# Performance work log

Hardware: AMD Instinct MI355X
Metric: run time of the kernel (lower is better)

## Reference

```python
import jax, jax.numpy as jnp
import numpy as np

DIM = 2048
N_HEADS = 16
HEAD_DIM = DIM // N_HEADS
HIDDEN = 8192
BATCH = 2
SEQ = 2048
EPS = 1e-6


def setup_inputs() -> dict:
    key = jax.random.key(0)
    ks = jax.random.split(key, 10)
    x = jax.random.normal(ks[0], (BATCH, SEQ, DIM), dtype=jnp.float32)
    # standard RoPE angles: theta_j = 10000^{-2j/head_dim}, angle = pos * theta_j
    inv_freq = 1.0 / (10000.0 ** (np.arange(0, HEAD_DIM, 2, dtype=np.float32) / HEAD_DIM))
    angles = np.arange(SEQ, dtype=np.float32)[:, None] * inv_freq[None, :]  # [S, HD/2]
    freqs_cos = jnp.asarray(np.cos(angles))
    freqs_sin = jnp.asarray(np.sin(angles))
    # causal mask added to scores
    mask = jnp.where(jnp.tril(jnp.ones((SEQ, SEQ), dtype=bool)), 0.0, -jnp.inf)[None, None].astype(jnp.float32)
    s = 0.02
    wq = jax.random.normal(ks[1], (DIM, DIM), jnp.float32) * s
    wk = jax.random.normal(ks[2], (DIM, DIM), jnp.float32) * s
    wv = jax.random.normal(ks[3], (DIM, DIM), jnp.float32) * s
    wo = jax.random.normal(ks[4], (DIM, DIM), jnp.float32) * s
    w1 = jax.random.normal(ks[5], (DIM, HIDDEN), jnp.float32) * s
    w2 = jax.random.normal(ks[6], (HIDDEN, DIM), jnp.float32) * s
    w3 = jax.random.normal(ks[7], (DIM, HIDDEN), jnp.float32) * s
    attn_norm_w = jnp.ones((DIM,), jnp.float32)
    ffn_norm_w = jnp.ones((DIM,), jnp.float32)
    return {"x": x, "freqs_cos": freqs_cos, "freqs_sin": freqs_sin, "mask": mask,
            "wq": wq, "wk": wk, "wv": wv, "wo": wo, "w1": w1, "w2": w2, "w3": w3,
            "attn_norm_w": attn_norm_w, "ffn_norm_w": ffn_norm_w}


def _rmsnorm(x, w):
    xf = x.astype(jnp.float32)
    y = xf * jax.lax.rsqrt(jnp.mean(xf * xf, axis=-1, keepdims=True) + EPS)
    return y.astype(x.dtype) * w


def _rope(t, cos, sin):
    # t: [B,S,H,HD]; complex mult on adjacent pairs
    tr = t.astype(jnp.float32).reshape(*t.shape[:-1], HEAD_DIM // 2, 2)
    a, b = tr[..., 0], tr[..., 1]
    c = cos[None, :, None, :]  # [1,S,1,HD/2]
    s = sin[None, :, None, :]
    out = jnp.stack([a * c - b * s, a * s + b * c], axis=-1)
    return out.reshape(t.shape).astype(t.dtype)


def reference(x, freqs_cos, freqs_sin, mask, wq, wk, wv, wo, w1, w2, w3, attn_norm_w, ffn_norm_w):
    B, S, D = x.shape
    xn = _rmsnorm(x, attn_norm_w)
    q = (xn @ wq).reshape(B, S, N_HEADS, HEAD_DIM)
    k = (xn @ wk).reshape(B, S, N_HEADS, HEAD_DIM)
    v = (xn @ wv).reshape(B, S, N_HEADS, HEAD_DIM)
    q = _rope(q, freqs_cos, freqs_sin)
    k = _rope(k, freqs_cos, freqs_sin)
    scale = 1.0 / jnp.sqrt(jnp.float32(HEAD_DIM))
    scores = jnp.einsum('bqhd,bkhd->bhqk', q, k) * scale + mask
    probs = jax.nn.softmax(scores.astype(jnp.float32), axis=-1).astype(q.dtype)
    attn = jnp.einsum('bhqk,bkhd->bqhd', probs, v).reshape(B, S, D)
    h = x + attn @ wo
    hn = _rmsnorm(h, ffn_norm_w)
    ff = (jax.nn.silu(hn @ w1) * (hn @ w3)) @ w2
    return h + ff
```

## Files before the change

### kernel.cpp

```cpp
#include <hip/hip_runtime.h>
#include <cmath>

#define DIM    2048
#define NHEADS 16
#define HD     128
#define HIDDEN 8192
#define SEQ    2048
#define MTOK   4096
#define EPS    1e-6f

typedef __bf16 bf16;
typedef __bf16 bf16x8 __attribute__((ext_vector_type(8)));
typedef __bf16 bf16x4 __attribute__((ext_vector_type(4)));
typedef float  f32x4  __attribute__((ext_vector_type(4)));

__global__ void k_transpose_bf16(const float* __restrict__ in, bf16* __restrict__ out,
                                 int R, int C) {
    __shared__ float tile[32][33];
    int r0 = blockIdx.y * 32, c0 = blockIdx.x * 32;
    int tx = threadIdx.x, ty = threadIdx.y;
#pragma unroll
    for (int i = ty; i < 32; i += 8)
        tile[i][tx] = in[(size_t)(r0 + i) * C + (c0 + tx)];
    __syncthreads();
#pragma unroll
    for (int i = ty; i < 32; i += 8)
        out[(size_t)(c0 + i) * R + (r0 + tx)] = (bf16)tile[tx][i];
}

__global__ void k_rmsnorm(const float* __restrict__ x, const float* __restrict__ w,
                          bf16* __restrict__ out) {
    int row = blockIdx.x;
    int tid = threadIdx.x;
    const float4* xr = (const float4*)(x + (size_t)row * DIM);
    float4 a = xr[tid];
    float4 b = xr[tid + 256];
    float ss = a.x*a.x + a.y*a.y + a.z*a.z + a.w*a.w
             + b.x*b.x + b.y*b.y + b.z*b.z + b.w*b.w;
#pragma unroll
    for (int off = 32; off > 0; off >>= 1) ss += __shfl_down(ss, off, 64);
    __shared__ float red[4];
    if ((tid & 63) == 0) red[tid >> 6] = ss;
    __syncthreads();
    float tot = red[0] + red[1] + red[2] + red[3];
    float inv = rsqrtf(tot * (1.0f / DIM) + EPS);
    const float4* wr = (const float4*)w;
    float4 w0 = wr[tid], w1 = wr[tid + 256];
    bf16x4* o = (bf16x4*)(out + (size_t)row * DIM);
    bf16x4 v0, v1;
    v0[0] = (bf16)(a.x * inv * w0.x); v0[1] = (bf16)(a.y * inv * w0.y);
    v0[2] = (bf16)(a.z * inv * w0.z); v0[3] = (bf16)(a.w * inv * w0.w);
    v1[0] = (bf16)(b.x * inv * w1.x); v1[1] = (bf16)(b.y * inv * w1.y);
    v1[2] = (bf16)(b.z * inv * w1.z); v1[3] = (bf16)(b.w * inv * w1.w);
    o[tid] = v0;
    o[tid + 256] = v1;
}

__global__ void k_rope(bf16* __restrict__ qb, bf16* __restrict__ kb,
                       const float* __restrict__ fcos, const float* __restrict__ fsin) {
    bf16* t = blockIdx.y ? kb : qb;
    int idx = blockIdx.x * 256 + threadIdx.x;
    int m = idx >> 10;
    int p = idx & 1023;
    int i = p & 63;
    int col = (p >> 6) * HD + 2 * i;
    int pos = m & (SEQ - 1);
    float c = fcos[pos * 64 + i], s = fsin[pos * 64 + i];
    size_t off = (size_t)m * DIM + col;
    float a = (float)t[off], b = (float)t[off + 1];
    t[off]     = (bf16)(a * c - b * s);
    t[off + 1] = (bf16)(a * s + b * c);
}

template<int DUAL, int RESID, int OUT_F32>
__global__ __launch_bounds__(256, 2) void k_gemm(
    const bf16* __restrict__ A, const bf16* __restrict__ B1,
    const bf16* __restrict__ B2, const float* __restrict__ resid,
    void* __restrict__ outp, int M, int N, int K)
{
    __shared__ bf16 As [128][72];
    __shared__ bf16 Bs1[128][72];
    __shared__ bf16 Bs2[DUAL ? 128 : 1][72];

    const int tid  = threadIdx.x;
    const int wid  = tid >> 6;
    const int lane = tid & 63;
    const int quad = lane >> 4;
    const int l16  = lane & 15;
    const int wm   = wid >> 1;
    const int wn   = wid & 1;
    const int m0   = blockIdx.y * 128;
    const int n0   = blockIdx.x * 128;
    const int tr   = tid >> 3;
    const int tc   = (tid & 7) * 8;

    f32x4 acc1[4][4] = {};
    f32x4 acc2[4][4] = {};

    const int nk = K >> 6;
    for (int kt = 0; kt < nk; ++kt) {
        const int k0 = kt << 6;
        __syncthreads();
#pragma unroll
        for (int p = 0; p < 4; ++p) {
            int row = p * 32 + tr;
            *(uint4*)&As [row][tc] = *(const uint4*)&A [(size_t)(m0 + row) * K + k0 + tc];
            *(uint4*)&Bs1[row][tc] = *(const uint4*)&B1[(size_t)(n0 + row) * K + k0 + tc];
            if (DUAL)
                *(uint4*)&Bs2[row][tc] = *(const uint4*)&B2[(size_t)(n0 + row) * K + k0 + tc];
        }
        __syncthreads();
#pragma unroll
        for (int kk = 0; kk < 64; kk += 32) {
            bf16x8 af[4], bf1[4], bf2[4];
#pragma unroll
            for (int i = 0; i < 4; ++i) {
                af[i]  = *(const bf16x8*)&As [wm * 64 + i * 16 + l16][kk + quad * 8];
                bf1[i] = *(const bf16x8*)&Bs1[wn * 64 + i * 16 + l16][kk + quad * 8];
                if (DUAL)
                    bf2[i] = *(const bf16x8*)&Bs2[wn * 64 + i * 16 + l16][kk + quad * 8];
            }
#pragma unroll
            for (int mi = 0; mi < 4; ++mi)
#pragma unroll
                for (int ni = 0; ni < 4; ++ni) {
                    acc1[mi][ni] = __builtin_amdgcn_mfma_f32_16x16x32_bf16(
                        af[mi], bf1[ni], acc1[mi][ni], 0, 0, 0);
                    if (DUAL)
                        acc2[mi][ni] = __builtin_amdgcn_mfma_f32_16x16x32_bf16(
                            af[mi], bf2[ni], acc2[mi][ni], 0, 0, 0);
                }
        }
    }

#pragma unroll
    for (int mi = 0; mi < 4; ++mi)
#pragma unroll
        for (int i = 0; i < 4; ++i) {
            int row = m0 + wm * 64 + mi * 16 + quad * 4 + i;
#pragma unroll
            for (int ni = 0; ni < 4; ++ni) {
                int col = n0 + wn * 64 + ni * 16 + l16;
                float v1 = acc1[mi][ni][i];
                if (DUAL) {
                    float v2 = acc2[mi][ni][i];
                    float g = v1 / (1.0f + __expf(-v1));
                    ((bf16*)outp)[(size_t)row * N + col] = (bf16)(g * v2);
                } else if (OUT_F32) {
                    float r = RESID ? resid[(size_t)row * N + col] : 0.0f;
                    ((float*)outp)[(size_t)row * N + col] = r + v1;
                } else {
                    ((bf16*)outp)[(size_t)row * N + col] = (bf16)v1;
                }
            }
        }
}

__global__ __launch_bounds__(256, 2) void k_flash(
    const bf16* __restrict__ q, const bf16* __restrict__ k,
    const bf16* __restrict__ v, bf16* __restrict__ o)
{
    const int qt = 15 - blockIdx.x;
    const int bh = blockIdx.y;
    const int b  = bh >> 4, h = bh & 15;
    const int tid  = threadIdx.x;
    const int wid  = tid >> 6, lane = tid & 63;
    const int quad = lane >> 4, l16 = lane & 15;

    __shared__ bf16 Ks [128][136];
    __shared__ bf16 Vts[128][136];

    const int q0 = qt * 128;
    const size_t baseQ  = ((size_t)b * SEQ + q0) * DIM + (size_t)h * HD;
    const size_t baseKV = ((size_t)b * SEQ) * DIM + (size_t)h * HD;

    bf16x8 qf[2][4];
#pragma unroll
    for (int mi = 0; mi < 2; ++mi)
#pragma unroll
        for (int ks = 0; ks < 4; ++ks)
            qf[mi][ks] = *(const bf16x8*)&q[baseQ +
                (size_t)(wid * 32 + mi * 16 + l16) * DIM + ks * 32 + quad * 8];

    f32x4 acc_o[2][8] = {};
    float m_run[2][4], l_run[2][4];
#pragma unroll
    for (int mi = 0; mi < 2; ++mi)
#pragma unroll
        for (int i = 0; i < 4; ++i) { m_run[mi][i] = -INFINITY; l_run[mi][i] = 0.f; }

    const float scale = 0.08838834764831845f;
    const int krow = tid >> 1, kcol = (tid & 1) * 64;

    for (int kt = 0; kt <= qt; ++kt) {
        const int kbase = kt * 128;
        __syncthreads();
#pragma unroll
        for (int j = 0; j < 8; ++j)
            *(uint4*)&Ks[krow][kcol + j * 8] =
                *(const uint4*)&k[baseKV + (size_t)(kbase + krow) * DIM + kcol + j * 8];
#pragma unroll
        for (int j = 0; j < 8; ++j) {
            bf16x8 vv = *(const bf16x8*)&v[baseKV + (size_t)(kbase + krow) * DIM + kcol + j * 8];
#pragma unroll
            for (int e = 0; e < 8; ++e)
                Vts[kcol + j * 8 + e][krow] = vv[e];
        }
        __syncthreads();

        f32x4 accs[2][8] = {};
#pragma unroll
        for (int ks = 0; ks < 4; ++ks)
#pragma unroll
            for (int ni = 0; ni < 8; ++ni) {
                bf16x8 kf = *(const bf16x8*)&Ks[ni * 16 + l16][ks * 32 + quad * 8];
#pragma unroll
                for (int mi = 0; mi < 2; ++mi)
                    accs[mi][ni] = __builtin_amdgcn_mfma_f32_16x16x32_bf16(
                        qf[mi][ks], kf, accs[mi][ni], 0, 0, 0);
            }

#pragma unroll
        for (int mi = 0; mi < 2; ++mi)
#pragma unroll
            for (int i = 0; i < 4; ++i) {
                int grow = q0 + wid * 32 + mi * 16 + quad * 4 + i;
                float mx = -INFINITY;
#pragma unroll
                for (int ni = 0; ni < 8; ++ni) {
                    float sv = accs[mi][ni][i] * scale;
                    int col = kbase + ni * 16 + l16;
                    if (col > grow) sv = -INFINITY;
                    accs[mi][ni][i] = sv;
                    mx = fmaxf(mx, sv);
                }
                mx = fmaxf(mx, __shfl_xor(mx, 1, 64));
                mx = fmaxf(mx, __shfl_xor(mx, 2, 64));
                mx = fmaxf(mx, __shfl_xor(mx, 4, 64));
                mx = fmaxf(mx, __shfl_xor(mx, 8, 64));
                float mnew  = fmaxf(m_run[mi][i], mx);
                float alpha = __expf(m_run[mi][i] - mnew);
                m_run[mi][i] = mnew;
                float rsum = 0.f;
#pragma unroll
                for (int ni = 0; ni < 8; ++ni) {
                    float p = __expf(accs[mi][ni][i] - mnew);
                    accs[mi][ni][i] = p;
                    rsum += p;
                }
                rsum += __shfl_xor(rsum, 1, 64);
                rsum += __shfl_xor(rsum, 2, 64);
                rsum += __shfl_xor(rsum, 4, 64);
                rsum += __shfl_xor(rsum, 8, 64);
                l_run[mi][i] = l_run[mi][i] * alpha + rsum;
#pragma unroll
                for (int ni = 0; ni < 8; ++ni) acc_o[mi][ni][i] *= alpha;
            }

        __syncthreads();
#pragma unroll
        for (int mi = 0; mi < 2; ++mi)
#pragma unroll
            for (int ni = 0; ni < 8; ++ni)
#pragma unroll
                for (int i = 0; i < 4; ++i)
                    Ks[wid * 32 + mi * 16 + quad * 4 + i][ni * 16 + l16] =
                        (bf16)accs[mi][ni][i];
        __syncthreads();

#pragma unroll
        for (int ks2 = 0; ks2 < 4; ++ks2) {
            bf16x8 pf[2];
#pragma unroll
            for (int mi = 0; mi < 2; ++mi)
                pf[mi] = *(const bf16x8*)&Ks[wid * 32 + mi * 16 + l16][ks2 * 32 + quad * 8];
#pragma unroll
            for (int ni = 0; ni < 8; ++ni) {
                bf16x8 vf = *(const bf16x8*)&Vts[ni * 16 + l16][ks2 * 32 + quad * 8];
#pragma unroll
                for (int mi = 0; mi < 2; ++mi)
                    acc_o[mi][ni] = __builtin_amdgcn_mfma_f32_16x16x32_bf16(
                        pf[mi], vf, acc_o[mi][ni], 0, 0, 0);
            }
        }
    }

#pragma unroll
    for (int mi = 0; mi < 2; ++mi)
#pragma unroll
        for (int i = 0; i < 4; ++i) {
            float invl = 1.0f / l_run[mi][i];
            int row = q0 + wid * 32 + mi * 16 + quad * 4 + i;
            size_t rb = ((size_t)b * SEQ + row) * DIM + (size_t)h * HD;
#pragma unroll
            for (int ni = 0; ni < 8; ++ni)
                o[rb + ni * 16 + l16] = (bf16)(acc_o[mi][ni][i] * invl);
        }
}

extern "C" void kernel_launch(void* const* d_in, const int* in_sizes, int n_in,
                              void* d_out, int out_size, void* d_ws, size_t ws_size,
                              hipStream_t stream)
{
    (void)in_sizes; (void)n_in; (void)out_size; (void)ws_size;
    const float* x    = (const float*)d_in[0];
    const float* fcos = (const float*)d_in[1];
    const float* fsin = (const float*)d_in[2];
    const float* wq   = (const float*)d_in[4];
    const float* wk   = (const float*)d_in[5];
    const float* wv   = (const float*)d_in[6];
    const float* wo   = (const float*)d_in[7];
    const float* w1   = (const float*)d_in[8];
    const float* w2   = (const float*)d_in[9];
    const float* w3   = (const float*)d_in[10];
    const float* anw  = (const float*)d_in[11];
    const float* fnw  = (const float*)d_in[12];
    float* out = (float*)d_out;

    char* ws = (char*)d_ws;
    size_t off = 0;
    auto alloc = [&](size_t bytes) { void* p = ws + off; off += (bytes + 255) & ~255ull; return p; };
    bf16* wqT = (bf16*)alloc((size_t)DIM * DIM * 2);
    bf16* wkT = (bf16*)alloc((size_t)DIM * DIM * 2);
    bf16* wvT = (bf16*)alloc((size_t)DIM * DIM * 2);
    bf16* woT = (bf16*)alloc((size_t)DIM * DIM * 2);
    bf16* w1T = (bf16*)alloc((size_t)HIDDEN * DIM * 2);
    bf16* w3T = (bf16*)alloc((size_t)HIDDEN * DIM * 2);
    bf16* xn  = (bf16*)alloc((size_t)MTOK * DIM * 2);
    bf16* qb  = (bf16*)alloc((size_t)MTOK * DIM * 2);
    bf16* kb  = (bf16*)alloc((size_t)MTOK * DIM * 2);
    bf16* vb  = (bf16*)alloc((size_t)MTOK * DIM * 2);
    bf16* ffb = (bf16*)alloc((size_t)MTOK * HIDDEN * 2);
    bf16* w2T = kb;

    dim3 tb(32, 8);
    k_transpose_bf16<<<dim3(DIM / 32, DIM / 32), tb, 0, stream>>>(wq, wqT, DIM, DIM);
    k_transpose_bf16<<<dim3(DIM / 32, DIM / 32), tb, 0, stream>>>(wk, wkT, DIM, DIM);
    k_transpose_bf16<<<dim3(DIM / 32, DIM / 32), tb, 0, stream>>>(wv, wvT, DIM, DIM);
    k_transpose_bf16<<<dim3(DIM / 32, DIM / 32), tb, 0, stream>>>(wo, woT, DIM, DIM);
    k_transpose_bf16<<<dim3(HIDDEN / 32, DIM / 32), tb, 0, stream>>>(w1, w1T, DIM, HIDDEN);
    k_transpose_bf16<<<dim3(HIDDEN / 32, DIM / 32), tb, 0, stream>>>(w3, w3T, DIM, HIDDEN);

    k_rmsnorm<<<MTOK, 256, 0, stream>>>(x, anw, xn);

    dim3 g2k(DIM / 128, MTOK / 128);
    k_gemm<0, 0, 0><<<g2k, 256, 0, stream>>>(xn, wqT, nullptr, nullptr, qb, MTOK, DIM, DIM);
    k_gemm<0, 0, 0><<<g2k, 256, 0, stream>>>(xn, wkT, nullptr, nullptr, kb, MTOK, DIM, DIM);
    k_gemm<0, 0, 0><<<g2k, 256, 0, stream>>>(xn, wvT, nullptr, nullptr, vb, MTOK, DIM, DIM);

    k_rope<<<dim3((MTOK * 1024) / 256, 2), 256, 0, stream>>>(qb, kb, fcos, fsin);

    k_flash<<<dim3(SEQ / 128, 2 * NHEADS), 256, 0, stream>>>(qb, kb, vb, qb);

    k_transpose_bf16<<<dim3(DIM / 32, HIDDEN / 32), tb, 0, stream>>>(w2, w2T, HIDDEN, DIM);

    k_gemm<0, 1, 1><<<g2k, 256, 0, stream>>>(qb, woT, nullptr, x, out, MTOK, DIM, DIM);

    k_rmsnorm<<<MTOK, 256, 0, stream>>>(out, fnw, xn);

    k_gemm<1, 0, 0><<<dim3(HIDDEN / 128, MTOK / 128), 256, 0, stream>>>(
        xn, w1T, w3T, nullptr, ffb, MTOK, HIDDEN, DIM);

    k_gemm<0, 1, 1><<<g2k, 256, 0, stream>>>(ffb, w2T, nullptr, out, out, MTOK, DIM, HIDDEN);
}
```

Baseline: 1.241 ms.

## Fuse QKV GEMMs with RoPE epilogue, use direct global-to-LDS loads in GEMM

Replaces the three separate Q/K/V GEMMs and the standalone RoPE kernel with one GEMM over the concatenated transposed weights. RoPE is applied in the epilogue, using a lane shuffle to pair adjacent columns. The GEMM tile loads now use global_load_lds to write straight into unpadded LDS, and launch bounds are raised to allow more resident blocks. The weight transpose moves to 64x64 tiles. This cuts launches, the extra read-modify-write pass over Q/K, and register staging, at the risk of LDS bank conflicts from the unpadded rows. It also relies on the Q/K/V weight buffers being contiguous in the workspace.

```diff
diff --git a/kernel.cpp b/kernel.cpp
--- a/kernel.cpp
+++ b/kernel.cpp
@@ -14,17 +14,22 @@
 typedef __bf16 bf16x4 __attribute__((ext_vector_type(4)));
 typedef float  f32x4  __attribute__((ext_vector_type(4)));
 
+__device__ __forceinline__ void gl_lds16(const void* g, void* l) {
+    __builtin_amdgcn_global_load_lds((const __attribute__((address_space(1))) void*)g,
+                                     (__attribute__((address_space(3))) void*)l, 16, 0, 0);
+}
+
 __global__ void k_transpose_bf16(const float* __restrict__ in, bf16* __restrict__ out,
                                  int R, int C) {
-    __shared__ float tile[32][33];
-    int r0 = blockIdx.y * 32, c0 = blockIdx.x * 32;
+    __shared__ float tile[64][65];
+    int r0 = blockIdx.y * 64, c0 = blockIdx.x * 64;
     int tx = threadIdx.x, ty = threadIdx.y;
 #pragma unroll
-    for (int i = ty; i < 32; i += 8)
+    for (int i = ty; i < 64; i += 4)
         tile[i][tx] = in[(size_t)(r0 + i) * C + (c0 + tx)];
     __syncthreads();
 #pragma unroll
-    for (int i = ty; i < 32; i += 8)
+    for (int i = ty; i < 64; i += 4)
         out[(size_t)(c0 + i) * R + (r0 + tx)] = (bf16)tile[tx][i];
 }
 
@@ -56,31 +61,18 @@
     o[tid + 256] = v1;
 }
 
-__global__ void k_rope(bf16* __restrict__ qb, bf16* __restrict__ kb,
-                       const float* __restrict__ fcos, const float* __restrict__ fsin) {
-    bf16* t = blockIdx.y ? kb : qb;
-    int idx = blockIdx.x * 256 + threadIdx.x;
-    int m = idx >> 10;
-    int p = idx & 1023;
-    int i = p & 63;
-    int col = (p >> 6) * HD + 2 * i;
-    int pos = m & (SEQ - 1);
-    float c = fcos[pos * 64 + i], s = fsin[pos * 64 + i];
-    size_t off = (size_t)m * DIM + col;
-    float a = (float)t[off], b = (float)t[off + 1];
-    t[off]     = (bf16)(a * c - b * s);
-    t[off + 1] = (bf16)(a * s + b * c);
-}
-
-template<int DUAL, int RESID, int OUT_F32>
-__global__ __launch_bounds__(256, 2) void k_gemm(
-    const bf16* __restrict__ A, const bf16* __restrict__ B1,
-    const bf16* __restrict__ B2, const float* __restrict__ resid,
-    void* __restrict__ outp, int M, int N, int K)
+template<int MODE>
+__global__ __launch_bounds__(256, MODE == 3 ? 3 : 4) void k_gemm(
+    const bf16* __restrict__ A, const bf16* __restrict__ B1, const bf16* __restrict__ B2,
+    const float* __restrict__ resid, const float* __restrict__ fcos,
+    const float* __restrict__ fsin,
+    bf16* __restrict__ oq, bf16* __restrict__ ok, bf16* __restrict__ ov,
+    float* __restrict__ of, int M, int N, int K)
 {
-    __shared__ bf16 As [128][72];
-    __shared__ bf16 Bs1[128][72];
-    __shared__ bf16 Bs2[DUAL ? 128 : 1][72];
+    __shared__ bf16 sm[(MODE == 3 ? 3 : 2) * 128 * 64];
+    bf16* As  = sm;
+    bf16* Bs1 = sm + 128 * 64;
+    bf16* Bs2 = sm + 2 * 128 * 64;
 
     const int tid  = threadIdx.x;
     const int wid  = tid >> 6;
@@ -91,8 +83,8 @@
     const int wn   = wid & 1;
     const int m0   = blockIdx.y * 128;
     const int n0   = blockIdx.x * 128;
-    const int tr   = tid >> 3;
-    const int tc   = (tid & 7) * 8;
+    const int lr   = lane >> 3;
+    const int lc   = (lane & 7) * 8;
 
     f32x4 acc1[4][4] = {};
     f32x4 acc2[4][4] = {};
@@ -102,12 +94,12 @@
         const int k0 = kt << 6;
         __syncthreads();
 #pragma unroll
-        for (int p = 0; p < 4; ++p) {
-            int row = p * 32 + tr;
-            *(uint4*)&As [row][tc] = *(const uint4*)&A [(size_t)(m0 + row) * K + k0 + tc];
-            *(uint4*)&Bs1[row][tc] = *(const uint4*)&B1[(size_t)(n0 + row) * K + k0 + tc];
-            if (DUAL)
-                *(uint4*)&Bs2[row][tc] = *(const uint4*)&B2[(size_t)(n0 + row) * K + k0 + tc];
+        for (int j = 0; j < 4; ++j) {
+            const int rb = wid * 32 + j * 8;
+            gl_lds16(&A [(size_t)(m0 + rb + lr) * K + k0 + lc], As  + rb * 64);
+            gl_lds16(&B1[(size_t)(n0 + rb + lr) * K + k0 + lc], Bs1 + rb * 64);
+            if (MODE == 3)
+                gl_lds16(&B2[(size_t)(n0 + rb + lr) * K + k0 + lc], Bs2 + rb * 64);
         }
         __syncthreads();
 #pragma unroll
@@ -115,10 +107,10 @@
             bf16x8 af[4], bf1[4], bf2[4];
 #pragma unroll
             for (int i = 0; i < 4; ++i) {
-                af[i]  = *(const bf16x8*)&As [wm * 64 + i * 16 + l16][kk + quad * 8];
-                bf1[i] = *(const bf16x8*)&Bs1[wn * 64 + i * 16 + l16][kk + quad * 8];
-                if (DUAL)
-                    bf2[i] = *(const bf16x8*)&Bs2[wn * 64 + i * 16 + l16][kk + quad * 8];
+                af[i]  = *(const bf16x8*)&As [(wm * 64 + i * 16 + l16) * 64 + kk + quad * 8];
+                bf1[i] = *(const bf16x8*)&Bs1[(wn * 64 + i * 16 + l16) * 64 + kk + quad * 8];
+                if (MODE == 3)
+                    bf2[i] = *(const bf16x8*)&Bs2[(wn * 64 + i * 16 + l16) * 64 + kk + quad * 8];
             }
 #pragma unroll
             for (int mi = 0; mi < 4; ++mi)
@@ -126,34 +118,56 @@
                 for (int ni = 0; ni < 4; ++ni) {
                     acc1[mi][ni] = __builtin_amdgcn_mfma_f32_16x16x32_bf16(
                         af[mi], bf1[ni], acc1[mi][ni], 0, 0, 0);
-                    if (DUAL)
+                    if (MODE == 3)
                         acc2[mi][ni] = __builtin_amdgcn_mfma_f32_16x16x32_bf16(
                             af[mi], bf2[ni], acc2[mi][ni], 0, 0, 0);
                 }
         }
     }
 
-#pragma unroll
-    for (int mi = 0; mi < 4; ++mi)
-#pragma unroll
-        for (int i = 0; i < 4; ++i) {
-            int row = m0 + wm * 64 + mi * 16 + quad * 4 + i;
-#pragma unroll
-            for (int ni = 0; ni < 4; ++ni) {
-                int col = n0 + wn * 64 + ni * 16 + l16;
-                float v1 = acc1[mi][ni][i];
-                if (DUAL) {
-                    float v2 = acc2[mi][ni][i];
-                    float g = v1 / (1.0f + __expf(-v1));
-                    ((bf16*)outp)[(size_t)row * N + col] = (bf16)(g * v2);
-                } else if (OUT_F32) {
-                    float r = RESID ? resid[(size_t)row * N + col] : 0.0f;
-                    ((float*)outp)[(size_t)row * N + col] = r + v1;
-                } else {
-                    ((bf16*)outp)[(size_t)row * N + col] = (bf16)v1;
-                }
-            }
-        }
+    if (MODE == 1) {
+        const int region = n0 >> 11;
+        bf16* dst = region == 0 ? oq : (region == 1 ? ok : ov);
+        const int c0 = (n0 & 2047) + wn * 64;
+#pragma unroll
+        for (int mi = 0; mi < 4; ++mi)
+#pragma unroll
+            for (int i = 0; i < 4; ++i) {
+                int row = m0 + wm * 64 + mi * 16 + quad * 4 + i;
+                int pos = row & (SEQ - 1);
+#pragma unroll
+                for (int ni = 0; ni < 4; ++ni) {
+                    int c = c0 + ni * 16 + l16;
+                    float vA = acc1[mi][ni][i];
+                    if (region < 2) {
+                        float vB = __shfl_xor(vA, 1, 64);
+                        int fi = (c & 127) >> 1;
+                        float cs = fcos[pos * 64 + fi], sn = fsin[pos * 64 + fi];
+                        vA = (l16 & 1) ? (vB * sn + vA * cs) : (vA * cs - vB * sn);
+                    }
+                    dst[(size_t)row * DIM + c] = (bf16)vA;
+                }
+            }
+    } else {
+#pragma unroll
+        for (int mi = 0; mi < 4; ++mi)
+#pragma unroll
+            for (int i = 0; i < 4; ++i) {
+                int row = m0 + wm * 64 + mi * 16 + quad * 4 + i;
+#pragma unroll
+                for (int ni = 0; ni < 4; ++ni) {
+                    int col = n0 + wn * 64 + ni * 16 + l16;
+                    float v1 = acc1[mi][ni][i];
+                    if (MODE == 3) {
+                        float v2 = acc2[mi][ni][i];
+                        float g = v1 / (1.0f + __expf(-v1));
+                        oq[(size_t)row * N + col] = (bf16)(g * v2);
+                    } else {
+                        of[(size_t)row * N + col] = resid[(size_t)row * N + col] + v1;
+                    }
+                }
+            }
+    }
 }
 
 __global__ __launch_bounds__(256, 2) void k_flash(
@@ -333,33 +347,33 @@
     bf16* ffb = (bf16*)alloc((size_t)MTOK * HIDDEN * 2);
     bf16* w2T = kb;
 
-    dim3 tb(32, 8);
-    k_transpose_bf16<<<dim3(DIM / 32, DIM / 32), tb, 0, stream>>>(wq, wqT, DIM, DIM);
-    k_transpose_bf16<<<dim3(DIM / 32, DIM / 32), tb, 0, stream>>>(wk, wkT, DIM, DIM);
-    k_transpose_bf16<<<dim3(DIM / 32, DIM / 32), tb, 0, stream>>>(wv, wvT, DIM, DIM);
-    k_transpose_bf16<<<dim3(DIM / 32, DIM / 32), tb, 0, stream>>>(wo, woT, DIM, DIM);
-    k_transpose_bf16<<<dim3(HIDDEN / 32, DIM / 32), tb, 0, stream>>>(w1, w1T, DIM, HIDDEN);
-    k_transpose_bf16<<<dim3(HIDDEN / 32, DIM / 32), tb, 0, stream>>>(w3, w3T, DIM, HIDDEN);
+    dim3 tb(64, 4);
+    k_transpose_bf16<<<dim3(DIM / 64, DIM / 64), tb, 0, stream>>>(wq, wqT, DIM, DIM);
+    k_transpose_bf16<<<dim3(DIM / 64, DIM / 64), tb, 0, stream>>>(wk, wkT, DIM, DIM);
+    k_transpose_bf16<<<dim3(DIM / 64, DIM / 64), tb, 0, stream>>>(wv, wvT, DIM, DIM);
+    k_transpose_bf16<<<dim3(DIM / 64, DIM / 64), tb, 0, stream>>>(wo, woT, DIM, DIM);
+    k_transpose_bf16<<<dim3(HIDDEN / 64, DIM / 64), tb, 0, stream>>>(w1, w1T, DIM, HIDDEN);
+    k_transpose_bf16<<<dim3(HIDDEN / 64, DIM / 64), tb, 0, stream>>>(w3, w3T, DIM, HIDDEN);
 
     k_rmsnorm<<<MTOK, 256, 0, stream>>>(x, anw, xn);
 
-    dim3 g2k(DIM / 128, MTOK / 128);
-    k_gemm<0, 0, 0><<<g2k, 256, 0, stream>>>(xn, wqT, nullptr, nullptr, qb, MTOK, DIM, DIM);
-    k_gemm<0, 0, 0><<<g2k, 256, 0, stream>>>(xn, wkT, nullptr, nullptr, kb, MTOK, DIM, DIM);
-    k_gemm<0, 0, 0><<<g2k, 256, 0, stream>>>(xn, wvT, nullptr, nullptr, vb, MTOK, DIM, DIM);
-
-    k_rope<<<dim3((MTOK * 1024) / 256, 2), 256, 0, stream>>>(qb, kb, fcos, fsin);
+    k_gemm<1><<<dim3(3 * DIM / 128, MTOK / 128), 256, 0, stream>>>(
+        xn, wqT, nullptr, nullptr, fcos, fsin, qb, kb, vb, nullptr, MTOK, 3 * DIM, DIM);
 
     k_flash<<<dim3(SEQ / 128, 2 * NHEADS), 256, 0, stream>>>(qb, kb, vb, qb);
 
-    k_transpose_bf16<<<dim3(DIM / 32, HIDDEN / 32), tb, 0, stream>>>(w2, w2T, HIDDEN, DIM);
-
-    k_gemm<0, 1, 1><<<g2k, 256, 0, stream>>>(qb, woT, nullptr, x, out, MTOK, DIM, DIM);
+    k_transpose_bf16<<<dim3(DIM / 64, HIDDEN / 64), tb, 0, stream>>>(w2, w2T, HIDDEN, DIM);
+
+    k_gemm<2><<<dim3(DIM / 128, MTOK / 128), 256, 0, stream>>>(
+        qb, woT, nullptr, x, nullptr, nullptr, nullptr, nullptr, nullptr, out, MTOK, DIM, DIM);
 
     k_rmsnorm<<<MTOK, 256, 0, stream>>>(out, fnw, xn);
 
-    k_gemm<1, 0, 0><<<dim3(HIDDEN / 128, MTOK / 128), 256, 0, stream>>>(
-        xn, w1T, w3T, nullptr, ffb, MTOK, HIDDEN, DIM);
-
-    k_gemm<0, 1, 1><<<g2k, 256, 0, stream>>>(ffb, w2T, nullptr, out, out, MTOK, DIM, HIDDEN);
-}
+    k_gemm<3><<<dim3(HIDDEN / 128, MTOK / 128), 256, 0, stream>>>(
+        xn, w1T, w3T, nullptr, nullptr, nullptr, ffb, nullptr, nullptr, nullptr,
+        MTOK, HIDDEN, DIM);
+
+    k_gemm<2><<<dim3(DIM / 128, MTOK / 128), 256, 0, stream>>>(
+        ffb, w2T, nullptr, out, nullptr, nullptr, nullptr, nullptr, nullptr, out,
+        MTOK, DIM, HIDDEN);
+}
```

Result: slower. 2.410 ms (+94.2%).
